# Optimization experiments

Hardware: AMD Instinct MI355X
Metric: run time of the kernel (lower is better)

## Reference

```python
import jax, jax.numpy as jnp
import numpy as np

D_MODEL = 1024
D_HIDDEN = 4096
NUM_EXPERTS = 8
TOP_K = 2


def setup_inputs() -> dict:
    key = jax.random.key(0)
    ks = jax.random.split(key, 7)
    scale_in = 1.0 / np.sqrt(D_MODEL)
    scale_hid = 1.0 / np.sqrt(D_HIDDEN)
    x = jax.random.normal(ks[0], (4, 2048, D_MODEL), dtype=jnp.float32)
    Wr = jax.random.uniform(ks[1], (D_MODEL, NUM_EXPERTS), jnp.float32, -scale_in, scale_in)
    br = jax.random.uniform(ks[2], (NUM_EXPERTS,), jnp.float32, -scale_in, scale_in)
    W1 = jax.random.uniform(ks[3], (NUM_EXPERTS, D_MODEL, D_HIDDEN), jnp.float32, -scale_in, scale_in)
    b1 = jax.random.uniform(ks[4], (NUM_EXPERTS, D_HIDDEN), jnp.float32, -scale_in, scale_in)
    W2 = jax.random.uniform(ks[5], (NUM_EXPERTS, D_HIDDEN, D_MODEL), jnp.float32, -scale_hid, scale_hid)
    b2 = jax.random.uniform(ks[6], (NUM_EXPERTS, D_MODEL), jnp.float32, -scale_hid, scale_hid)
    return {"x": x, "Wr": Wr, "br": br, "W1": W1, "b1": b1, "W2": W2, "b2": b2}


def reference(x, Wr, br, W1, b1, W2, b2):
    B, S, D = x.shape
    E = Wr.shape[1]
    flat = x.reshape(-1, D)                      # [T, D]
    T = flat.shape[0]
    logits = flat @ Wr + br                      # [T, E]
    probs = jax.nn.softmax(logits, axis=-1)
    topk_p, topk_i = jax.lax.top_k(probs, TOP_K)  # [T, K]
    topk_p = topk_p / jnp.sum(topk_p, axis=-1, keepdims=True)
    # combine[t, e] = sum_k topk_p[t, k] * (topk_i[t, k] == e)
    combine = jnp.zeros((T, E), flat.dtype).at[jnp.arange(T)[:, None], topk_i].add(topk_p)
    out = jnp.zeros_like(flat)
    for e in range(E):  # fixed small expert loop; each iter is a dense GEMM pair
        h = jax.nn.relu(flat @ W1[e] + b1[e])    # [T, d_hidden]
        y = h @ W2[e] + b2[e]                    # [T, D]
        out = out + y * combine[:, e:e + 1]
    return out.reshape(B, S, D)
```

## Files before the change

kernel.cpp:

```cpp
#include <hip/hip_runtime.h>
#include <stdint.h>

#define D_MODEL  1024
#define D_HIDDEN 4096
#define NE       8
#define T_TOK    8192
#define BM       128
#define BN       128
#define BK       64
#define MAXT     136
#define ROWS_CAP 17408

typedef __attribute__((ext_vector_type(8))) short short8;
typedef __attribute__((ext_vector_type(4))) float f32x4;

__device__ inline uint16_t f2bf(float f) {
  uint32_t u = __float_as_uint(f);
  uint32_t r = (u + 0x7fffu + ((u >> 16) & 1u)) >> 16;
  return (uint16_t)r;
}

#define GLOAD16(gp, lp) __builtin_amdgcn_global_load_lds( \
  (const __attribute__((address_space(1))) uint32_t*)(gp), \
  (__attribute__((address_space(3))) uint32_t*)(lp), 16, 0, 0)

__global__ void transpose_cvt(const float* __restrict__ in, uint16_t* __restrict__ out,
                              int R, int C) {
  __shared__ float tile[32][33];
  size_t eoff = (size_t)blockIdx.z * R * C;
  in += eoff; out += eoff;
  int c0 = blockIdx.x * 32, r0 = blockIdx.y * 32;
  int x = threadIdx.x, y = threadIdx.y;
#pragma unroll
  for (int i = 0; i < 32; i += 8)
    tile[y + i][x] = in[(size_t)(r0 + y + i) * C + c0 + x];
  __syncthreads();
#pragma unroll
  for (int i = 0; i < 32; i += 8)
    out[(size_t)(c0 + y + i) * R + r0 + x] = f2bf(tile[x][y + i]);
}

__global__ void router_kernel(const float* __restrict__ x, const float* __restrict__ Wr,
                              const float* __restrict__ br,
                              int* __restrict__ cnt, int* __restrict__ tok_of,
                              int* __restrict__ k_of, float* __restrict__ tok_w) {
  int t = blockIdx.x * 4 + (threadIdx.x >> 6);
  int l = threadIdx.x & 63;
  const float* xr = x + (size_t)t * D_MODEL;
  float a[8] = {0.f,0.f,0.f,0.f,0.f,0.f,0.f,0.f};
  for (int d = l; d < D_MODEL; d += 64) {
    float xv = xr[d];
    const float4* w4 = (const float4*)(Wr + d * 8);
    float4 wa = w4[0], wb = w4[1];
    a[0] += xv * wa.x; a[1] += xv * wa.y; a[2] += xv * wa.z; a[3] += xv * wa.w;
    a[4] += xv * wb.x; a[5] += xv * wb.y; a[6] += xv * wb.z; a[7] += xv * wb.w;
  }
#pragma unroll
  for (int e = 0; e < 8; ++e) {
    float v = a[e];
#pragma unroll
    for (int off = 32; off > 0; off >>= 1) v += __shfl_xor(v, off);
    a[e] = v + br[e];
  }
  if (l == 0) {
    int i1 = 0; float v1 = a[0];
#pragma unroll
    for (int e = 1; e < 8; ++e) if (a[e] > v1) { v1 = a[e]; i1 = e; }
    int i2 = -1; float v2 = -1e30f;
#pragma unroll
    for (int e = 0; e < 8; ++e) if (e != i1 && a[e] > v2) { v2 = a[e]; i2 = e; }
    float e2 = __expf(v2 - v1);
    float inv = 1.0f / (1.0f + e2);
    int p1 = atomicAdd(cnt + i1, 1);
    tok_of[i1 * T_TOK + p1] = t; k_of[i1 * T_TOK + p1] = 0;
    int p2 = atomicAdd(cnt + i2, 1);
    tok_of[i2 * T_TOK + p2] = t; k_of[i2 * T_TOK + p2] = 1;
    tok_w[t * 2 + 0] = inv; tok_w[t * 2 + 1] = e2 * inv;
  }
}

__global__ void setup_kernel(const int* __restrict__ cnt, int* __restrict__ meta) {
  if (threadIdx.x != 0 || blockIdx.x != 0) return;
  int base = 0, nt = 0;
  meta[1] = 0;
  for (int e = 0; e < NE; ++e) {
    int c = cnt[e];
    int tiles = (c + BM - 1) / BM;
    for (int i = 0; i < tiles; ++i) {
      meta[16 + nt] = e;
      meta[16 + MAXT + nt] = base + i * BM;
      nt++;
    }
    base += tiles * BM;
    meta[2 + e] = base;
  }
  meta[0] = nt;
}

__global__ void gather_kernel(const float* __restrict__ x, const int* __restrict__ cnt,
                              const int* __restrict__ meta, const int* __restrict__ tok_of,
                              const int* __restrict__ k_of,
                              uint16_t* __restrict__ xp, int* __restrict__ tok2row) {
  int r = blockIdx.x * 4 + (threadIdx.x >> 6);
  int l = threadIdx.x & 63;
  int total = meta[9];
  if (r >= total) return;
  int e = 0;
#pragma unroll
  for (int i = 1; i < 8; ++i) if (r >= meta[1 + i]) e = i;
  int p = r - meta[1 + e];
  uint16_t* dst = xp + (size_t)r * D_MODEL + l * 16;
  if (p < cnt[e]) {
    int t = tok_of[e * T_TOK + p];
    if (l == 0) tok2row[t * 2 + k_of[e * T_TOK + p]] = r;
    const float4* src = (const float4*)(x + (size_t)t * D_MODEL + l * 16);
    short8 o0, o1;
    float4 v0 = src[0], v1 = src[1], v2 = src[2], v3 = src[3];
    o0[0] = (short)f2bf(v0.x); o0[1] = (short)f2bf(v0.y);
    o0[2] = (short)f2bf(v0.z); o0[3] = (short)f2bf(v0.w);
    o0[4] = (short)f2bf(v1.x); o0[5] = (short)f2bf(v1.y);
    o0[6] = (short)f2bf(v1.z); o0[7] = (short)f2bf(v1.w);
    o1[0] = (short)f2bf(v2.x); o1[1] = (short)f2bf(v2.y);
    o1[2] = (short)f2bf(v2.z); o1[3] = (short)f2bf(v2.w);
    o1[4] = (short)f2bf(v3.x); o1[5] = (short)f2bf(v3.y);
    o1[6] = (short)f2bf(v3.z); o1[7] = (short)f2bf(v3.w);
    *(short8*)dst = o0;
    *(short8*)(dst + 8) = o1;
  } else {
    short8 z = {0,0,0,0,0,0,0,0};
    *(short8*)dst = z;
    *(short8*)(dst + 8) = z;
  }
}

template<int KD, int ND, bool RELU_BF16>
__global__ void moe_gemm(const uint16_t* __restrict__ A, const uint16_t* __restrict__ Bt,
                         const float* __restrict__ bias,
                         uint16_t* __restrict__ Cb, float* __restrict__ Cf,
                         const int* __restrict__ meta) {
  int nt = meta[0];
  int mt = blockIdx.y;
  if (mt >= nt) return;
  int e = meta[16 + mt];
  int row0 = meta[16 + MAXT + mt];
  int n0 = blockIdx.x * BN;

  __shared__ __align__(16) uint16_t lA[BM * BK];
  __shared__ __align__(16) uint16_t lB[BN * BK];

  int t = threadIdx.x;
  int w = t >> 6, l = t & 63;
  int wr = (w >> 1) * 64, wc = (w & 1) * 64;

  const uint16_t* Ab = A + (size_t)row0 * KD;
  const uint16_t* Bb = Bt + ((size_t)e * ND + n0) * KD;

  f32x4 acc[4][4];
#pragma unroll
  for (int m = 0; m < 4; ++m)
#pragma unroll
    for (int n = 0; n < 4; ++n) acc[m][n] = (f32x4){0.f, 0.f, 0.f, 0.f};

  int trow = t >> 3;
  int tcol = (t & 7) * 8;

  for (int kt = 0; kt < KD / BK; ++kt) {
    int k0 = kt * BK;
    __syncthreads();
#pragma unroll
    for (int i = 0; i < 4; ++i) {
      GLOAD16(Ab + (size_t)(i * 32 + trow) * KD + k0 + tcol, lA + (i * 32 + trow) * BK + tcol);
      GLOAD16(Bb + (size_t)(i * 32 + trow) * KD + k0 + tcol, lB + (i * 32 + trow) * BK + tcol);
    }
    asm volatile("s_waitcnt vmcnt(0)" ::: "memory");
    __syncthreads();
#pragma unroll
    for (int kk = 0; kk < 2; ++kk) {
      short8 af[4], bf[4];
      int ko = kk * 32 + (l >> 4) * 8;
#pragma unroll
      for (int m = 0; m < 4; ++m)
        af[m] = *(const short8*)(lA + (wr + m * 16 + (l & 15)) * BK + ko);
#pragma unroll
      for (int n = 0; n < 4; ++n)
        bf[n] = *(const short8*)(lB + (wc + n * 16 + (l & 15)) * BK + ko);
#pragma unroll
      for (int m = 0; m < 4; ++m)
#pragma unroll
        for (int n = 0; n < 4; ++n)
          acc[m][n] = __builtin_amdgcn_mfma_f32_16x16x32_bf16(af[m], bf[n], acc[m][n], 0, 0, 0);
    }
  }

#pragma unroll
  for (int m = 0; m < 4; ++m) {
    int row_b = row0 + wr + m * 16 + (l >> 4) * 4;
#pragma unroll
    for (int n = 0; n < 4; ++n) {
      int col = n0 + wc + n * 16 + (l & 15);
      float bv = bias[e * ND + col];
#pragma unroll
      for (int r = 0; r < 4; ++r) {
        float v = acc[m][n][r] + bv;
        size_t off = (size_t)(row_b + r) * ND + col;
        if (RELU_BF16) Cb[off] = f2bf(fmaxf(v, 0.f));
        else           Cf[off] = v;
      }
    }
  }
}

__global__ void combine_kernel(const float* __restrict__ y, const int* __restrict__ tok2row,
                               const float* __restrict__ tok_w, float* __restrict__ out) {
  int t = blockIdx.x;
  int i = threadIdx.x;
  int r0 = tok2row[t * 2], r1 = tok2row[t * 2 + 1];
  float w0 = tok_w[t * 2], w1 = tok_w[t * 2 + 1];
  float4 av = ((const float4*)(y + (size_t)r0 * D_MODEL))[i];
  float4 bv = ((const float4*)(y + (size_t)r1 * D_MODEL))[i];
  float4 res;
  res.x = w0 * av.x + w1 * bv.x;
  res.y = w0 * av.y + w1 * bv.y;
  res.z = w0 * av.z + w1 * bv.z;
  res.w = w0 * av.w + w1 * bv.w;
  ((float4*)(out + (size_t)t * D_MODEL))[i] = res;
}

extern "C" void kernel_launch(void* const* d_in, const int* in_sizes, int n_in,
                              void* d_out, int out_size, void* d_ws, size_t ws_size,
                              hipStream_t stream) {
  const float* x  = (const float*)d_in[0];
  const float* Wr = (const float*)d_in[1];
  const float* br = (const float*)d_in[2];
  const float* W1 = (const float*)d_in[3];
  const float* b1 = (const float*)d_in[4];
  const float* W2 = (const float*)d_in[5];
  const float* b2 = (const float*)d_in[6];
  float* out = (float*)d_out;

  char* ws = (char*)d_ws;
  size_t off = 0;
  auto alloc = [&](size_t bytes) -> void* {
    void* p = ws + off;
    off += (bytes + 255) & ~(size_t)255;
    return p;
  };
  uint16_t* W1T   = (uint16_t*)alloc((size_t)NE * D_MODEL * D_HIDDEN * 2);
  uint16_t* W2T   = (uint16_t*)alloc((size_t)NE * D_MODEL * D_HIDDEN * 2);
  uint16_t* xp    = (uint16_t*)alloc((size_t)ROWS_CAP * D_MODEL * 2);
  uint16_t* hp    = (uint16_t*)alloc((size_t)ROWS_CAP * D_HIDDEN * 2);
  float*    y     = (float*)alloc((size_t)ROWS_CAP * D_MODEL * 4);
  int*      cnt   = (int*)alloc(NE * 4);
  int*      tok_of= (int*)alloc((size_t)NE * T_TOK * 4);
  int*      k_of  = (int*)alloc((size_t)NE * T_TOK * 4);
  float*    tok_w = (float*)alloc(T_TOK * 2 * 4);
  int*      t2r   = (int*)alloc(T_TOK * 2 * 4);
  int*      meta  = (int*)alloc((16 + 2 * MAXT) * 4);

  if (ws_size < off) return;

  hipMemsetAsync(cnt, 0, NE * 4, stream);
  transpose_cvt<<<dim3(D_HIDDEN / 32, D_MODEL / 32, NE), dim3(32, 8), 0, stream>>>(
      W1, W1T, D_MODEL, D_HIDDEN);
  transpose_cvt<<<dim3(D_MODEL / 32, D_HIDDEN / 32, NE), dim3(32, 8), 0, stream>>>(
      W2, W2T, D_HIDDEN, D_MODEL);
  router_kernel<<<T_TOK / 4, 256, 0, stream>>>(x, Wr, br, cnt, tok_of, k_of, tok_w);
  setup_kernel<<<1, 64, 0, stream>>>(cnt, meta);
  gather_kernel<<<ROWS_CAP / 4, 256, 0, stream>>>(x, cnt, meta, tok_of, k_of, xp, t2r);
  moe_gemm<D_MODEL, D_HIDDEN, true><<<dim3(D_HIDDEN / BN, MAXT), 256, 0, stream>>>(
      xp, W1T, b1, hp, nullptr, meta);
  moe_gemm<D_HIDDEN, D_MODEL, false><<<dim3(D_MODEL / BN, MAXT), 256, 0, stream>>>(
      hp, W2T, b2, nullptr, y, meta);
  combine_kernel<<<T_TOK, 256, 0, stream>>>(y, t2r, tok_w, out);
}
```

Measured before the change: 730.3 us.

## Double-buffer MoE GEMM with swizzled LDS and fuse weighted combine via atomics

Rewrites the expert GEMM main loop as a double-buffered pipeline. The next k-slice is prefetched with global_load_lds while MFMAs run on the current one, using an XOR-swizzled LDS layout to avoid bank conflicts and raised wave priority around the MFMA block. The second GEMM's epilogue now scales its results by the routing weight and atomically adds them into the zeroed output, which removes the fp32 y buffer and the separate combine kernel. The gather kernel now records row-to-token and row-weight maps in place of token-to-row. The trade-offs are float atomics, which make summation order nondeterministic, and an extra memset of the output.

```diff
diff --git a/kernel.cpp b/kernel.cpp
--- a/kernel.cpp
+++ b/kernel.cpp
@@ -7,7 +7,6 @@
 #define T_TOK    8192
 #define BM       128
 #define BN       128
-#define BK       64
 #define MAXT     136
 #define ROWS_CAP 17408
 
@@ -99,8 +98,9 @@
 
 __global__ void gather_kernel(const float* __restrict__ x, const int* __restrict__ cnt,
                               const int* __restrict__ meta, const int* __restrict__ tok_of,
-                              const int* __restrict__ k_of,
-                              uint16_t* __restrict__ xp, int* __restrict__ tok2row) {
+                              const int* __restrict__ k_of, const float* __restrict__ tok_w,
+                              uint16_t* __restrict__ xp,
+                              int* __restrict__ row2tok, float* __restrict__ row2w) {
   int r = blockIdx.x * 4 + (threadIdx.x >> 6);
   int l = threadIdx.x & 63;
   int total = meta[9];
@@ -112,7 +112,10 @@
   uint16_t* dst = xp + (size_t)r * D_MODEL + l * 16;
   if (p < cnt[e]) {
     int t = tok_of[e * T_TOK + p];
-    if (l == 0) tok2row[t * 2 + k_of[e * T_TOK + p]] = r;
+    if (l == 0) {
+      row2tok[r] = t;
+      row2w[r] = tok_w[t * 2 + k_of[e * T_TOK + p]];
+    }
     const float4* src = (const float4*)(x + (size_t)t * D_MODEL + l * 16);
     short8 o0, o1;
     float4 v0 = src[0], v1 = src[1], v2 = src[2], v3 = src[3];
@@ -127,17 +130,19 @@
     *(short8*)dst = o0;
     *(short8*)(dst + 8) = o1;
   } else {
+    if (l == 0) { row2tok[r] = -1; row2w[r] = 0.f; }
     short8 z = {0,0,0,0,0,0,0,0};
     *(short8*)dst = z;
     *(short8*)(dst + 8) = z;
   }
 }
 
-template<int KD, int ND, bool RELU_BF16>
-__global__ void moe_gemm(const uint16_t* __restrict__ A, const uint16_t* __restrict__ Bt,
-                         const float* __restrict__ bias,
-                         uint16_t* __restrict__ Cb, float* __restrict__ Cf,
-                         const int* __restrict__ meta) {
+template<int KD, int ND, bool FUSED_OUT>
+__global__ __launch_bounds__(256, 2) void moe_gemm(
+    const uint16_t* __restrict__ A, const uint16_t* __restrict__ Bt,
+    const float* __restrict__ bias, uint16_t* __restrict__ Cb,
+    float* __restrict__ out, const int* __restrict__ row2tok,
+    const float* __restrict__ row2w, const int* __restrict__ meta) {
   int nt = meta[0];
   int mt = blockIdx.y;
   if (mt >= nt) return;
@@ -145,12 +150,19 @@
   int row0 = meta[16 + MAXT + mt];
   int n0 = blockIdx.x * BN;
 
-  __shared__ __align__(16) uint16_t lA[BM * BK];
-  __shared__ __align__(16) uint16_t lB[BN * BK];
-
-  int t = threadIdx.x;
-  int w = t >> 6, l = t & 63;
-  int wr = (w >> 1) * 64, wc = (w & 1) * 64;
+  __shared__ __align__(16) uint16_t L[32768];
+
+  int tid = threadIdx.x;
+  int l = tid & 63, w = tid >> 6;
+  int wrow = w >> 1, wcol = w & 1;
+  int arow_r = wrow * 64 + (l & 15);
+  int brow_r = wcol * 64 + (l & 15);
+  int koff = ((l >> 4) ^ ((l >> 1) & 3)) * 8;
+
+  int r0s = tid >> 2;
+  int sseg = (tid & 3) ^ ((r0s >> 1) & 3);
+  size_t goA0 = (size_t)r0s * KD + sseg * 8;
+  size_t goA1 = (size_t)(r0s + 64) * KD + sseg * 8;
 
   const uint16_t* Ab = A + (size_t)row0 * KD;
   const uint16_t* Bb = Bt + ((size_t)e * ND + n0) * KD;
@@ -161,69 +173,91 @@
 #pragma unroll
     for (int n = 0; n < 4; ++n) acc[m][n] = (f32x4){0.f, 0.f, 0.f, 0.f};
 
-  int trow = t >> 3;
-  int tcol = (t & 7) * 8;
-
-  for (int kt = 0; kt < KD / BK; ++kt) {
-    int k0 = kt * BK;
-    __syncthreads();
-#pragma unroll
-    for (int i = 0; i < 4; ++i) {
-      GLOAD16(Ab + (size_t)(i * 32 + trow) * KD + k0 + tcol, lA + (i * 32 + trow) * BK + tcol);
-      GLOAD16(Bb + (size_t)(i * 32 + trow) * KD + k0 + tcol, lB + (i * 32 + trow) * BK + tcol);
-    }
-    asm volatile("s_waitcnt vmcnt(0)" ::: "memory");
-    __syncthreads();
-#pragma unroll
-    for (int kk = 0; kk < 2; ++kk) {
-      short8 af[4], bf[4];
-      int ko = kk * 32 + (l >> 4) * 8;
-#pragma unroll
-      for (int m = 0; m < 4; ++m)
-        af[m] = *(const short8*)(lA + (wr + m * 16 + (l & 15)) * BK + ko);
-#pragma unroll
-      for (int n = 0; n < 4; ++n)
-        bf[n] = *(const short8*)(lB + (wc + n * 16 + (l & 15)) * BK + ko);
-#pragma unroll
-      for (int m = 0; m < 4; ++m)
-#pragma unroll
-        for (int n = 0; n < 4; ++n)
-          acc[m][n] = __builtin_amdgcn_mfma_f32_16x16x32_bf16(af[m], bf[n], acc[m][n], 0, 0, 0);
-    }
-  }
-
-#pragma unroll
-  for (int m = 0; m < 4; ++m) {
-    int row_b = row0 + wr + m * 16 + (l >> 4) * 4;
-#pragma unroll
-    for (int n = 0; n < 4; ++n) {
-      int col = n0 + wc + n * 16 + (l & 15);
-      float bv = bias[e * ND + col];
-#pragma unroll
-      for (int r = 0; r < 4; ++r) {
-        float v = acc[m][n][r] + bv;
-        size_t off = (size_t)(row_b + r) * ND + col;
-        if (RELU_BF16) Cb[off] = f2bf(fmaxf(v, 0.f));
-        else           Cf[off] = v;
+  auto stage = [&](int buf, int kh, int kt) {
+    const uint16_t* ga = Ab + kt * 64 + kh * 32;
+    const uint16_t* gb = Bb + kt * 64 + kh * 32;
+    uint16_t* lb = L + buf * 16384 + kh * 8192;
+    GLOAD16(ga + goA0, lb + tid * 8);
+    GLOAD16(ga + goA1, lb + 2048 + tid * 8);
+    GLOAD16(gb + goA0, lb + 4096 + tid * 8);
+    GLOAD16(gb + goA1, lb + 6144 + tid * 8);
+  };
+
+#define PHASE(BUF, KK, DO_STAGE, NKT, VM) do {                                  \
+    short8 af[4], bf[4];                                                        \
+    const uint16_t* Lb = L + (BUF) * 16384 + (KK) * 8192;                       \
+    _Pragma("unroll") for (int m = 0; m < 4; ++m)                               \
+      af[m] = *(const short8*)(Lb + (arow_r + m * 16) * 32 + koff);             \
+    _Pragma("unroll") for (int n = 0; n < 4; ++n)                               \
+      bf[n] = *(const short8*)(Lb + 4096 + (brow_r + n * 16) * 32 + koff);      \
+    if (DO_STAGE) stage((BUF) ^ 1, (KK), (NKT));                                \
+    asm volatile("s_waitcnt vmcnt(" #VM ")" ::: "memory");                      \
+    __builtin_amdgcn_s_barrier();                                               \
+    asm volatile("s_waitcnt lgkmcnt(0)" ::: "memory");                          \
+    __builtin_amdgcn_sched_barrier(0);                                          \
+    __builtin_amdgcn_s_setprio(1);                                              \
+    _Pragma("unroll") for (int m = 0; m < 4; ++m)                               \
+      _Pragma("unroll") for (int n = 0; n < 4; ++n)                             \
+        acc[m][n] = __builtin_amdgcn_mfma_f32_16x16x32_bf16(af[m], bf[n],       \
+                                                            acc[m][n], 0, 0, 0);\
+    __builtin_amdgcn_s_setprio(0);                                              \
+    __builtin_amdgcn_s_barrier();                                               \
+  } while (0)
+
+  constexpr int NT = KD / 64;
+  stage(0, 0, 0);
+  stage(0, 1, 0);
+  asm volatile("s_waitcnt vmcnt(4)" ::: "memory");
+  __builtin_amdgcn_s_barrier();
+
+  int t = 0;
+  for (; t + 2 < NT; t += 2) {
+    PHASE(0, 0, true, t + 1, 4);
+    PHASE(0, 1, true, t + 1, 4);
+    PHASE(1, 0, true, t + 2, 4);
+    PHASE(1, 1, true, t + 2, 4);
+  }
+  PHASE(0, 0, true, NT - 1, 4);
+  PHASE(0, 1, true, NT - 1, 4);
+  PHASE(1, 0, false, 0, 0);
+  PHASE(1, 1, false, 0, 0);
+#undef PHASE
+
+  float bv[4];
+#pragma unroll
+  for (int n = 0; n < 4; ++n)
+    bv[n] = bias[e * ND + n0 + wcol * 64 + n * 16 + (l & 15)];
+
+  if (!FUSED_OUT) {
+#pragma unroll
+    for (int m = 0; m < 4; ++m) {
+      int row_b = row0 + wrow * 64 + m * 16 + (l >> 4) * 4;
+#pragma unroll
+      for (int n = 0; n < 4; ++n) {
+        int col = n0 + wcol * 64 + n * 16 + (l & 15);
+#pragma unroll
+        for (int r = 0; r < 4; ++r)
+          Cb[(size_t)(row_b + r) * ND + col] = f2bf(fmaxf(acc[m][n][r] + bv[n], 0.f));
       }
     }
-  }
-}
-
-__global__ void combine_kernel(const float* __restrict__ y, const int* __restrict__ tok2row,
-                               const float* __restrict__ tok_w, float* __restrict__ out) {
-  int t = blockIdx.x;
-  int i = threadIdx.x;
-  int r0 = tok2row[t * 2], r1 = tok2row[t * 2 + 1];
-  float w0 = tok_w[t * 2], w1 = tok_w[t * 2 + 1];
-  float4 av = ((const float4*)(y + (size_t)r0 * D_MODEL))[i];
-  float4 bv = ((const float4*)(y + (size_t)r1 * D_MODEL))[i];
-  float4 res;
-  res.x = w0 * av.x + w1 * bv.x;
-  res.y = w0 * av.y + w1 * bv.y;
-  res.z = w0 * av.z + w1 * bv.z;
-  res.w = w0 * av.w + w1 * bv.w;
-  ((float4*)(out + (size_t)t * D_MODEL))[i] = res;
+  } else {
+#pragma unroll
+    for (int m = 0; m < 4; ++m) {
+#pragma unroll
+      for (int r = 0; r < 4; ++r) {
+        int grow = row0 + wrow * 64 + m * 16 + (l >> 4) * 4 + r;
+        int tok = row2tok[grow];
+        float wgt = row2w[grow];
+        if (tok >= 0) {
+#pragma unroll
+          for (int n = 0; n < 4; ++n) {
+            int col = n0 + wcol * 64 + n * 16 + (l & 15);
+            atomicAdd(out + (size_t)tok * ND + col, wgt * (acc[m][n][r] + bv[n]));
+          }
+        }
+      }
+    }
+  }
 }
 
 extern "C" void kernel_launch(void* const* d_in, const int* in_sizes, int n_in,
@@ -245,31 +279,32 @@
     off += (bytes + 255) & ~(size_t)255;
     return p;
   };
-  uint16_t* W1T   = (uint16_t*)alloc((size_t)NE * D_MODEL * D_HIDDEN * 2);
-  uint16_t* W2T   = (uint16_t*)alloc((size_t)NE * D_MODEL * D_HIDDEN * 2);
-  uint16_t* xp    = (uint16_t*)alloc((size_t)ROWS_CAP * D_MODEL * 2);
-  uint16_t* hp    = (uint16_t*)alloc((size_t)ROWS_CAP * D_HIDDEN * 2);
-  float*    y     = (float*)alloc((size_t)ROWS_CAP * D_MODEL * 4);
-  int*      cnt   = (int*)alloc(NE * 4);
-  int*      tok_of= (int*)alloc((size_t)NE * T_TOK * 4);
-  int*      k_of  = (int*)alloc((size_t)NE * T_TOK * 4);
-  float*    tok_w = (float*)alloc(T_TOK * 2 * 4);
-  int*      t2r   = (int*)alloc(T_TOK * 2 * 4);
-  int*      meta  = (int*)alloc((16 + 2 * MAXT) * 4);
+  uint16_t* W1T    = (uint16_t*)alloc((size_t)NE * D_MODEL * D_HIDDEN * 2);
+  uint16_t* W2T    = (uint16_t*)alloc((size_t)NE * D_MODEL * D_HIDDEN * 2);
+  uint16_t* xp     = (uint16_t*)alloc((size_t)ROWS_CAP * D_MODEL * 2);
+  uint16_t* hp     = (uint16_t*)alloc((size_t)ROWS_CAP * D_HIDDEN * 2);
+  int*      cnt    = (int*)alloc(NE * 4);
+  int*      tok_of = (int*)alloc((size_t)NE * T_TOK * 4);
+  int*      k_of   = (int*)alloc((size_t)NE * T_TOK * 4);
+  float*    tok_w  = (float*)alloc(T_TOK * 2 * 4);
+  int*      row2tok= (int*)alloc(ROWS_CAP * 4);
+  float*    row2w  = (float*)alloc(ROWS_CAP * 4);
+  int*      meta   = (int*)alloc((16 + 2 * MAXT) * 4);
 
   if (ws_size < off) return;
 
   hipMemsetAsync(cnt, 0, NE * 4, stream);
+  hipMemsetAsync(out, 0, (size_t)out_size * 4, stream);
   transpose_cvt<<<dim3(D_HIDDEN / 32, D_MODEL / 32, NE), dim3(32, 8), 0, stream>>>(
       W1, W1T, D_MODEL, D_HIDDEN);
   transpose_cvt<<<dim3(D_MODEL / 32, D_HIDDEN / 32, NE), dim3(32, 8), 0, stream>>>(
       W2, W2T, D_HIDDEN, D_MODEL);
   router_kernel<<<T_TOK / 4, 256, 0, stream>>>(x, Wr, br, cnt, tok_of, k_of, tok_w);
   setup_kernel<<<1, 64, 0, stream>>>(cnt, meta);
-  gather_kernel<<<ROWS_CAP / 4, 256, 0, stream>>>(x, cnt, meta, tok_of, k_of, xp, t2r);
-  moe_gemm<D_MODEL, D_HIDDEN, true><<<dim3(D_HIDDEN / BN, MAXT), 256, 0, stream>>>(
-      xp, W1T, b1, hp, nullptr, meta);
-  moe_gemm<D_HIDDEN, D_MODEL, false><<<dim3(D_MODEL / BN, MAXT), 256, 0, stream>>>(
-      hp, W2T, b2, nullptr, y, meta);
-  combine_kernel<<<T_TOK, 256, 0, stream>>>(y, t2r, tok_w, out);
-}
+  gather_kernel<<<ROWS_CAP / 4, 256, 0, stream>>>(x, cnt, meta, tok_of, k_of, tok_w,
+                                                  xp, row2tok, row2w);
+  moe_gemm<D_MODEL, D_HIDDEN, false><<<dim3(D_HIDDEN / BN, MAXT), 256, 0, stream>>>(
+      xp, W1T, b1, hp, nullptr, nullptr, nullptr, meta);
+  moe_gemm<D_HIDDEN, D_MODEL, true><<<dim3(D_MODEL / BN, MAXT), 256, 0, stream>>>(
+      hp, W2T, b2, nullptr, out, row2tok, row2w, meta);
+}
```

Result: slower. 746.4 us (+2.2%).
